# Kernel tuning notes

Hardware: AMD Instinct MI355X
Metric: run time of the kernel (lower is better)

Reference implementation:

```python
import jax, jax.numpy as jnp
import numpy as np

N_NODES = 40000
N_EDGES = 640000
D_IN = 128
D_OUT = 128
LN_EPS = 1e-5


def setup_inputs() -> dict:
    key = jax.random.key(0)
    ks = jax.random.split(key, 8)
    x = jax.random.normal(ks[0], (N_NODES, D_IN), dtype=jnp.float32)
    edge_index = jax.random.randint(ks[1], (2, N_EDGES), 0, N_NODES, dtype=jnp.int64)
    edge_weight_mean = jax.random.normal(ks[2], (N_EDGES,), dtype=jnp.float32)
    edge_weight_var = jax.random.uniform(ks[3], (N_EDGES,), dtype=jnp.float32)
    s = 1.0 / np.sqrt(D_IN)
    W_mean = jax.random.normal(ks[4], (D_IN, D_OUT), dtype=jnp.float32) * s
    b_mean = jax.random.normal(ks[5], (D_OUT,), dtype=jnp.float32) * 0.01
    W_logvar = jax.random.normal(ks[6], (D_IN, D_OUT), dtype=jnp.float32) * s
    b_logvar = jax.random.normal(ks[7], (D_OUT,), dtype=jnp.float32) * 0.01
    gamma = jnp.ones((D_OUT,), dtype=jnp.float32)
    beta = jnp.zeros((D_OUT,), dtype=jnp.float32)
    return {"x": x, "edge_index": edge_index, "edge_weight_mean": edge_weight_mean,
            "edge_weight_var": edge_weight_var, "W_mean": W_mean, "b_mean": b_mean,
            "W_logvar": W_logvar, "b_logvar": b_logvar, "gamma": gamma, "beta": beta}


def reference(x, edge_index, edge_weight_mean, edge_weight_var,
              W_mean, b_mean, W_logvar, b_logvar, gamma, beta):
    num_nodes = x.shape[0]
    h_mean = x @ W_mean + b_mean                      # [N, C]
    h_var = jnp.exp(x @ W_logvar + b_logvar)          # [N, C]
    row, col = edge_index[0], edge_index[1]
    ewm = edge_weight_mean[:, None]                   # [E, 1]
    ewv = edge_weight_var[:, None]                    # [E, 1]
    hm_c = h_mean[col]                                # gather [E, C]
    hv_c = h_var[col]
    msg_mean = hm_c * ewm
    msg_var = ewm ** 2 * hv_c + hm_c ** 2 * ewv
    out_mean = jax.ops.segment_sum(msg_mean, row, num_segments=num_nodes)
    out_var = jax.ops.segment_sum(msg_var, row, num_segments=num_nodes)
    degree = jax.ops.segment_sum(jnp.ones_like(edge_weight_mean), row, num_segments=num_nodes)
    degree = jnp.clip(degree, 1.0)[:, None]
    out_mean = out_mean / degree
    out_var = out_var / degree ** 2
    # LayerNorm over last dim (dropout is identity in eval mode)
    mu = jnp.mean(out_mean, axis=-1, keepdims=True)
    var = jnp.mean((out_mean - mu) ** 2, axis=-1, keepdims=True)
    out_mean = (out_mean - mu) * jax.lax.rsqrt(var + LN_EPS) * gamma + beta
    return (out_mean, out_var)
```

## Files before the change

kernel.cpp:

```cpp
#include <hip/hip_runtime.h>
#include <hip/hip_bf16.h>
#include <math.h>

#define N_NODES 40000
#define N_EDGES 640000
#define D 128
#define LN_EPS 1e-5f
#define STRIDE 48

typedef __attribute__((ext_vector_type(8))) short bf16x8;
typedef __attribute__((ext_vector_type(4))) float f32x4;

__device__ __forceinline__ unsigned bf2pack(float a, float b) {
    unsigned ua = __float_as_uint(a);
    ua = (ua + 0x7fffu + ((ua >> 16) & 1u)) >> 16;
    unsigned ub = __float_as_uint(b);
    ub = (ub + 0x7fffu + ((ub >> 16) & 1u)) >> 16;
    return ua | (ub << 16);
}
__device__ __forceinline__ unsigned short bfr(float a) {
    unsigned ua = __float_as_uint(a);
    return (unsigned short)((ua + 0x7fffu + ((ua >> 16) & 1u)) >> 16);
}
__device__ __forceinline__ float bflo(unsigned u) { return __uint_as_float(u << 16); }
__device__ __forceinline__ float bfhi(unsigned u) { return __uint_as_float(u & 0xffff0000u); }

__global__ __launch_bounds__(256) void packw_kernel(
    const float* __restrict__ Wm, const float* __restrict__ Wv,
    const float* __restrict__ bm, const float* __restrict__ bv,
    unsigned short* __restrict__ Wpk, float* __restrict__ bcat,
    int* __restrict__ counts)
{
    int idx = blockIdx.x * 256 + threadIdx.x;
    if (idx < N_NODES) counts[idx] = 0;
    if (idx < 256) bcat[idx] = (idx < 128) ? bm[idx] : bv[idx - 128];
    if (idx >= 32768) return;
    int j  = idx & 7;
    int l  = (idx >> 3) & 63;
    int nt = (idx >> 9) & 15;
    int kt = idx >> 13;
    int k = kt * 32 + (l >> 4) * 8 + j;
    int c = nt * 16 + (l & 15);
    float w = (c < 128) ? Wm[k * 128 + c] : Wv[k * 128 + (c - 128)];
    Wpk[idx] = bfr(w);
}

__global__ __launch_bounds__(256) void gemm_kernel(
    const float* __restrict__ x, const unsigned short* __restrict__ Wpk,
    const float* __restrict__ bcat, unsigned* __restrict__ hb,
    const int* __restrict__ row, int* __restrict__ counts,
    int* __restrict__ rank)
{
    const int gid = blockIdx.x * 256 + threadIdx.x;
    int4 r = ((const int4*)row)[gid];
    int k0 = atomicAdd(&counts[r.x], 1);
    int k1 = atomicAdd(&counts[r.y], 1);
    int k2 = atomicAdd(&counts[r.z], 1);
    int k3 = atomicAdd(&counts[r.w], 1);

    {
        const int w = threadIdx.x >> 6;
        const int l = threadIdx.x & 63;
        const int rbase = blockIdx.x * 64 + w * 16;
        const int arow = rbase + (l & 15);
        const int kqo = (l >> 4) * 8;

        bf16x8 a[4];
        #pragma unroll
        for (int kt = 0; kt < 4; ++kt) {
            const float* ap = &x[(size_t)arow * 128 + kt * 32 + kqo];
            float4 lo = *(const float4*)ap;
            float4 hi = *(const float4*)(ap + 4);
            uint4 au;
            au.x = bf2pack(lo.x, lo.y); au.y = bf2pack(lo.z, lo.w);
            au.z = bf2pack(hi.x, hi.y); au.w = bf2pack(hi.z, hi.w);
            a[kt] = *(bf16x8*)&au;
        }

        f32x4 acc[16];
        #pragma unroll
        for (int nt = 0; nt < 16; ++nt) acc[nt] = (f32x4){0.f, 0.f, 0.f, 0.f};

        const bf16x8* wp = (const bf16x8*)Wpk;
        #pragma unroll
        for (int kt = 0; kt < 4; ++kt) {
            #pragma unroll
            for (int nt = 0; nt < 16; ++nt) {
                bf16x8 b = wp[(kt * 16 + nt) * 64 + l];
                acc[nt] = __builtin_amdgcn_mfma_f32_16x16x32_bf16(a[kt], b, acc[nt], 0, 0, 0);
            }
        }

        const int c0 = l & 15;
        const int rq = rbase + (l >> 4) * 4;
        #pragma unroll
        for (int nt = 0; nt < 8; ++nt) {
            float bmv = bcat[nt * 16 + c0];
            float bvv = bcat[128 + nt * 16 + c0];
            #pragma unroll
            for (int q = 0; q < 4; ++q) {
                float m = acc[nt][q] + bmv;
                float v = expf(acc[nt + 8][q] + bvv);
                hb[(size_t)(rq + q) * 128 + nt * 16 + c0] = bf2pack(m, v);
            }
        }
    }

    ((int4*)rank)[gid] = make_int4(k0, k1, k2, k3);
}

__global__ __launch_bounds__(256) void scatter_kernel(
    const int* __restrict__ row, const int* __restrict__ col,
    const float* __restrict__ ewm, const float* __restrict__ ewv,
    const int* __restrict__ rank, uint2* __restrict__ ep8)
{
    int gid = blockIdx.x * 256 + threadIdx.x;
    int4   r  = ((const int4*)row)[gid];
    int4   c  = ((const int4*)col)[gid];
    int4   k  = ((const int4*)rank)[gid];
    float4 wm = ((const float4*)ewm)[gid];
    float4 wv = ((const float4*)ewv)[gid];

    if (k.x < STRIDE) ep8[(size_t)r.x * STRIDE + k.x] =
        make_uint2((unsigned)c.x, bf2pack(wm.x, wv.x));
    if (k.y < STRIDE) ep8[(size_t)r.y * STRIDE + k.y] =
        make_uint2((unsigned)c.y, bf2pack(wm.y, wv.y));
    if (k.z < STRIDE) ep8[(size_t)r.z * STRIDE + k.z] =
        make_uint2((unsigned)c.z, bf2pack(wm.z, wv.z));
    if (k.w < STRIDE) ep8[(size_t)r.w * STRIDE + k.w] =
        make_uint2((unsigned)c.w, bf2pack(wm.w, wv.w));
}

__device__ __forceinline__ void accum_edge(
    const uint4& h, float wm, float wv, float (&am)[4], float (&av)[4])
{
    float wm2 = wm * wm;
    float mf, vf;
    mf = bflo(h.x); vf = bfhi(h.x);
    am[0] = fmaf(mf, wm, am[0]);
    av[0] = fmaf(wm2, vf, fmaf(mf * mf, wv, av[0]));
    mf = bflo(h.y); vf = bfhi(h.y);
    am[1] = fmaf(mf, wm, am[1]);
    av[1] = fmaf(wm2, vf, fmaf(mf * mf, wv, av[1]));
    mf = bflo(h.z); vf = bfhi(h.z);
    am[2] = fmaf(mf, wm, am[2]);
    av[2] = fmaf(wm2, vf, fmaf(mf * mf, wv, av[2]));
    mf = bflo(h.w); vf = bfhi(h.w);
    am[3] = fmaf(mf, wm, am[3]);
    av[3] = fmaf(wm2, vf, fmaf(mf * mf, wv, av[3]));
}

__global__ __launch_bounds__(256) void agg_kernel(
    const uint4* __restrict__ hb, const int* __restrict__ counts,
    const uint2* __restrict__ ep8,
    const float* __restrict__ gamma, const float* __restrict__ beta,
    float* __restrict__ out)
{
    const int wid  = threadIdx.x >> 6;
    const int lane = threadIdx.x & 63;
    const int half = lane >> 5;
    const int sub  = lane & 31;
    const int n = blockIdx.x * 4 + wid;

    const int start = n * STRIDE;
    int cnt = counts[n];
    const int end = start + (cnt < STRIDE ? cnt : STRIDE);

    float am[4] = {}, av[4] = {};

    int e = start;
    for (; e + 8 <= end; e += 8) {
        uint2 m[4]; uint4 h[4];
        #pragma unroll
        for (int i = 0; i < 4; ++i) m[i] = ep8[e + 2 * i + half];
        #pragma unroll
        for (int i = 0; i < 4; ++i)
            h[i] = hb[(size_t)m[i].x * 32 + sub];
        #pragma unroll
        for (int i = 0; i < 4; ++i)
            accum_edge(h[i], bflo(m[i].y), bfhi(m[i].y), am, av);
    }
    for (; e + 2 <= end; e += 2) {
        uint2 m = ep8[e + half];
        uint4 h = hb[(size_t)m.x * 32 + sub];
        accum_edge(h, bflo(m.y), bfhi(m.y), am, av);
    }
    if (e < end && half == 0) {
        uint2 m = ep8[e];
        uint4 h = hb[(size_t)m.x * 32 + sub];
        accum_edge(h, bflo(m.y), bfhi(m.y), am, av);
    }

    #pragma unroll
    for (int j = 0; j < 4; ++j) {
        am[j] += __shfl_xor(am[j], 32);
        av[j] += __shfl_xor(av[j], 32);
    }

    float degi = 1.0f / fmaxf((float)(end - start), 1.0f);
    float dg2 = degi * degi;
    #pragma unroll
    for (int j = 0; j < 4; ++j) { am[j] *= degi; av[j] *= dg2; }

    float s = am[0] + am[1] + am[2] + am[3];
    #pragma unroll
    for (int off = 16; off >= 1; off >>= 1) s += __shfl_xor(s, off);
    float mu = s * (1.0f / 128.0f);
    float d0 = am[0] - mu, d1 = am[1] - mu, d2 = am[2] - mu, d3 = am[3] - mu;
    float q = d0 * d0 + d1 * d1 + d2 * d2 + d3 * d3;
    #pragma unroll
    for (int off = 16; off >= 1; off >>= 1) q += __shfl_xor(q, off);
    float var = q * (1.0f / 128.0f);
    float rs = rsqrtf(var + LN_EPS);

    if (half == 0) {
        float4 g = *(const float4*)&gamma[sub * 4];
        float4 b = *(const float4*)&beta[sub * 4];
        float4 om = make_float4(fmaf(d0 * rs, g.x, b.x), fmaf(d1 * rs, g.y, b.y),
                                fmaf(d2 * rs, g.z, b.z), fmaf(d3 * rs, g.w, b.w));
        *(float4*)&out[(size_t)n * D + sub * 4] = om;
        *(float4*)&out[(size_t)N_NODES * D + (size_t)n * D + sub * 4] =
            make_float4(av[0], av[1], av[2], av[3]);
    }
}

extern "C" void kernel_launch(void* const* d_in, const int* in_sizes, int n_in,
                              void* d_out, int out_size, void* d_ws, size_t ws_size,
                              hipStream_t stream)
{
    const float* x     = (const float*)d_in[0];
    const int*   eidx  = (const int*)d_in[1];
    const float* ewm   = (const float*)d_in[2];
    const float* ewv   = (const float*)d_in[3];
    const float* Wm    = (const float*)d_in[4];
    const float* bm    = (const float*)d_in[5];
    const float* Wv    = (const float*)d_in[6];
    const float* bv    = (const float*)d_in[7];
    const float* gamma = (const float*)d_in[8];
    const float* beta  = (const float*)d_in[9];
    const int* row = eidx;
    const int* col = eidx + N_EDGES;

    char* ws = (char*)d_ws;
    size_t off = 0;
    auto alloc = [&](size_t bytes) {
        void* p = ws + off;
        off += (bytes + 255) & ~(size_t)255;
        return p;
    };
    unsigned* hb        = (unsigned*)alloc((size_t)N_NODES * 512);
    unsigned short* Wpk = (unsigned short*)alloc(32768 * 2);
    float* bcat    = (float*)alloc(256 * 4);
    int*   counts  = (int*)alloc((size_t)N_NODES * 4);
    int*   rank    = (int*)alloc((size_t)N_EDGES * 4);
    uint2* ep8     = (uint2*)alloc((size_t)N_NODES * STRIDE * 8);

    packw_kernel<<<160, 256, 0, stream>>>(Wm, Wv, bm, bv, Wpk, bcat, counts);
    gemm_kernel<<<N_NODES / 64, 256, 0, stream>>>(x, Wpk, bcat, hb, row, counts, rank);
    scatter_kernel<<<N_EDGES / 4 / 256, 256, 0, stream>>>(
        row, col, ewm, ewv, rank, ep8);
    agg_kernel<<<N_NODES / 4, 256, 0, stream>>>(
        (const uint4*)hb, counts, ep8, gamma, beta, (float*)d_out);
}
```

Baseline: 105.7 us.

## Slice feature table by 16-column blocks and split aggregation from LayerNorm

The packed h table is stored transposed into 8 feature slices, each holding 16 columns for every node. Aggregation now runs one grid block per (node group, slice), so each slice's gather working set (about 2.5 MB) can stay in cache. LayerNorm moves to a separate kernel that rereads the mean output. The cost is 8x more edge-list reads, 4-byte instead of 16-byte gathers, and an extra launch plus an extra round trip of the mean output through memory.

```diff
diff --git a/kernel.cpp b/kernel.cpp
--- a/kernel.cpp
+++ b/kernel.cpp
@@ -47,7 +47,7 @@
 
 __global__ __launch_bounds__(256) void gemm_kernel(
     const float* __restrict__ x, const unsigned short* __restrict__ Wpk,
-    const float* __restrict__ bcat, unsigned* __restrict__ hb,
+    const float* __restrict__ bcat, unsigned* __restrict__ hbT,
     const int* __restrict__ row, int* __restrict__ counts,
     int* __restrict__ rank)
 {
@@ -101,7 +101,8 @@
             for (int q = 0; q < 4; ++q) {
                 float m = acc[nt][q] + bmv;
                 float v = expf(acc[nt + 8][q] + bvv);
-                hb[(size_t)(rq + q) * 128 + nt * 16 + c0] = bf2pack(m, v);
+                hbT[(size_t)nt * (N_NODES * 16) + (size_t)(rq + q) * 16 + c0] =
+                    bf2pack(m, v);
             }
         }
     }
@@ -131,97 +132,71 @@
         make_uint2((unsigned)c.w, bf2pack(wm.w, wv.w));
 }
 
-__device__ __forceinline__ void accum_edge(
-    const uint4& h, float wm, float wv, float (&am)[4], float (&av)[4])
-{
-    float wm2 = wm * wm;
-    float mf, vf;
-    mf = bflo(h.x); vf = bfhi(h.x);
-    am[0] = fmaf(mf, wm, am[0]);
-    av[0] = fmaf(wm2, vf, fmaf(mf * mf, wv, av[0]));
-    mf = bflo(h.y); vf = bfhi(h.y);
-    am[1] = fmaf(mf, wm, am[1]);
-    av[1] = fmaf(wm2, vf, fmaf(mf * mf, wv, av[1]));
-    mf = bflo(h.z); vf = bfhi(h.z);
-    am[2] = fmaf(mf, wm, am[2]);
-    av[2] = fmaf(wm2, vf, fmaf(mf * mf, wv, av[2]));
-    mf = bflo(h.w); vf = bfhi(h.w);
-    am[3] = fmaf(mf, wm, am[3]);
-    av[3] = fmaf(wm2, vf, fmaf(mf * mf, wv, av[3]));
-}
-
-__global__ __launch_bounds__(256) void agg_kernel(
-    const uint4* __restrict__ hb, const int* __restrict__ counts,
-    const uint2* __restrict__ ep8,
+__global__ __launch_bounds__(256) void aggA_kernel(
+    const unsigned* __restrict__ hbT, const int* __restrict__ counts,
+    const uint2* __restrict__ ep8, float* __restrict__ out)
+{
+    const int wv   = threadIdx.x >> 6;
+    const int lane = threadIdx.x & 63;
+    const int fl   = lane & 15;
+    const int eg   = lane >> 4;
+    const int slice = blockIdx.x & 7;
+    const int n = (blockIdx.x >> 3) * 4 + wv;
+
+    const int start = n * STRIDE;
+    int cnt = counts[n];
+    cnt = cnt < STRIDE ? cnt : STRIDE;
+    const int end = start + cnt;
+
+    const unsigned* hs = hbT + (size_t)slice * (N_NODES * 16);
+
+    float am = 0.f, av = 0.f;
+    for (int e = start + eg; e < end; e += 4) {
+        uint2 m = ep8[e];
+        unsigned h = hs[(size_t)m.x * 16 + fl];
+        float hm = bflo(h), hv = bfhi(h);
+        float wm = bflo(m.y), wvv = bfhi(m.y);
+        am = fmaf(hm, wm, am);
+        av = fmaf(wm * wm, hv, fmaf(hm * hm, wvv, av));
+    }
+    am += __shfl_xor(am, 16); am += __shfl_xor(am, 32);
+    av += __shfl_xor(av, 16); av += __shfl_xor(av, 32);
+
+    float degi = 1.0f / fmaxf((float)cnt, 1.0f);
+    am *= degi;
+    av *= degi * degi;
+
+    if (eg == 0) {
+        int feat = slice * 16 + fl;
+        out[(size_t)n * D + feat] = am;
+        out[(size_t)N_NODES * D + (size_t)n * D + feat] = av;
+    }
+}
+
+__global__ __launch_bounds__(256) void aggB_kernel(
     const float* __restrict__ gamma, const float* __restrict__ beta,
     float* __restrict__ out)
 {
-    const int wid  = threadIdx.x >> 6;
+    const int wv = threadIdx.x >> 6;
     const int lane = threadIdx.x & 63;
-    const int half = lane >> 5;
-    const int sub  = lane & 31;
-    const int n = blockIdx.x * 4 + wid;
-
-    const int start = n * STRIDE;
-    int cnt = counts[n];
-    const int end = start + (cnt < STRIDE ? cnt : STRIDE);
-
-    float am[4] = {}, av[4] = {};
-
-    int e = start;
-    for (; e + 8 <= end; e += 8) {
-        uint2 m[4]; uint4 h[4];
-        #pragma unroll
-        for (int i = 0; i < 4; ++i) m[i] = ep8[e + 2 * i + half];
-        #pragma unroll
-        for (int i = 0; i < 4; ++i)
-            h[i] = hb[(size_t)m[i].x * 32 + sub];
-        #pragma unroll
-        for (int i = 0; i < 4; ++i)
-            accum_edge(h[i], bflo(m[i].y), bfhi(m[i].y), am, av);
-    }
-    for (; e + 2 <= end; e += 2) {
-        uint2 m = ep8[e + half];
-        uint4 h = hb[(size_t)m.x * 32 + sub];
-        accum_edge(h, bflo(m.y), bfhi(m.y), am, av);
-    }
-    if (e < end && half == 0) {
-        uint2 m = ep8[e];
-        uint4 h = hb[(size_t)m.x * 32 + sub];
-        accum_edge(h, bflo(m.y), bfhi(m.y), am, av);
-    }
-
+    const int n = blockIdx.x * 4 + wv;
+
+    float2 a = *(const float2*)&out[(size_t)n * D + lane * 2];
+    float s = a.x + a.y;
     #pragma unroll
-    for (int j = 0; j < 4; ++j) {
-        am[j] += __shfl_xor(am[j], 32);
-        av[j] += __shfl_xor(av[j], 32);
-    }
-
-    float degi = 1.0f / fmaxf((float)(end - start), 1.0f);
-    float dg2 = degi * degi;
+    for (int off = 32; off >= 1; off >>= 1) s += __shfl_xor(s, off);
+    float mu = s * (1.0f / 128.0f);
+    float d0 = a.x - mu, d1 = a.y - mu;
+    float q = d0 * d0 + d1 * d1;
     #pragma unroll
-    for (int j = 0; j < 4; ++j) { am[j] *= degi; av[j] *= dg2; }
-
-    float s = am[0] + am[1] + am[2] + am[3];
-    #pragma unroll
-    for (int off = 16; off >= 1; off >>= 1) s += __shfl_xor(s, off);
-    float mu = s * (1.0f / 128.0f);
-    float d0 = am[0] - mu, d1 = am[1] - mu, d2 = am[2] - mu, d3 = am[3] - mu;
-    float q = d0 * d0 + d1 * d1 + d2 * d2 + d3 * d3;
-    #pragma unroll
-    for (int off = 16; off >= 1; off >>= 1) q += __shfl_xor(q, off);
+    for (int off = 32; off >= 1; off >>= 1) q += __shfl_xor(q, off);
     float var = q * (1.0f / 128.0f);
     float rs = rsqrtf(var + LN_EPS);
 
-    if (half == 0) {
-        float4 g = *(const float4*)&gamma[sub * 4];
-        float4 b = *(const float4*)&beta[sub * 4];
-        float4 om = make_float4(fmaf(d0 * rs, g.x, b.x), fmaf(d1 * rs, g.y, b.y),
-                                fmaf(d2 * rs, g.z, b.z), fmaf(d3 * rs, g.w, b.w));
-        *(float4*)&out[(size_t)n * D + sub * 4] = om;
-        *(float4*)&out[(size_t)N_NODES * D + (size_t)n * D + sub * 4] =
-            make_float4(av[0], av[1], av[2], av[3]);
-    }
+    float2 g = *(const float2*)&gamma[lane * 2];
+    float2 b = *(const float2*)&beta[lane * 2];
+    *(float2*)&out[(size_t)n * D + lane * 2] =
+        make_float2(fmaf(d0 * rs, g.x, b.x), fmaf(d1 * rs, g.y, b.y));
 }
 
 extern "C" void kernel_launch(void* const* d_in, const int* in_sizes, int n_in,
@@ -248,7 +223,7 @@
         off += (bytes + 255) & ~(size_t)255;
         return p;
     };
-    unsigned* hb        = (unsigned*)alloc((size_t)N_NODES * 512);
+    unsigned* hbT       = (unsigned*)alloc((size_t)N_NODES * 512);
     unsigned short* Wpk = (unsigned short*)alloc(32768 * 2);
     float* bcat    = (float*)alloc(256 * 4);
     int*   counts  = (int*)alloc((size_t)N_NODES * 4);
@@ -256,9 +231,10 @@
     uint2* ep8     = (uint2*)alloc((size_t)N_NODES * STRIDE * 8);
 
     packw_kernel<<<160, 256, 0, stream>>>(Wm, Wv, bm, bv, Wpk, bcat, counts);
-    gemm_kernel<<<N_NODES / 64, 256, 0, stream>>>(x, Wpk, bcat, hb, row, counts, rank);
+    gemm_kernel<<<N_NODES / 64, 256, 0, stream>>>(x, Wpk, bcat, hbT, row, counts, rank);
     scatter_kernel<<<N_EDGES / 4 / 256, 256, 0, stream>>>(
         row, col, ewm, ewv, rank, ep8);
-    agg_kernel<<<N_NODES / 4, 256, 0, stream>>>(
-        (const uint4*)hb, counts, ep8, gamma, beta, (float*)d_out);
-}
+    aggA_kernel<<<(N_NODES / 4) * 8, 256, 0, stream>>>(
+        hbT, counts, ep8, (float*)d_out);
+    aggB_kernel<<<N_NODES / 4, 256, 0, stream>>>(gamma, beta, (float*)d_out);
+}
```

New measurement: 204.7 us. +93.6%, slower.

## Fuse edge scatter into GEMM kernel and store fp32 edge weights in float4 packs

Applied to the files above, without the earlier changes.

The separate scatter kernel is folded into the GEMM kernel: each thread now handles two edges, takes their slot ranks via atomics and immediately writes the CSR-like edge record, so the rank buffer round trip and one launch disappear. The GEMM grid is doubled to 1250 blocks of 32 rows, with each wave computing half of the output columns for both mean and logvar. Edge records grow from 8-byte packed bf16 to 16-byte float4 with full-precision weights, which doubles the edge traffic in the aggregation kernel but removes the bf16 rounding of the weights.

```diff
diff --git a/kernel.cpp b/kernel.cpp
--- a/kernel.cpp
+++ b/kernel.cpp
@@ -48,20 +48,20 @@
 __global__ __launch_bounds__(256) void gemm_kernel(
     const float* __restrict__ x, const unsigned short* __restrict__ Wpk,
     const float* __restrict__ bcat, unsigned* __restrict__ hb,
-    const int* __restrict__ row, int* __restrict__ counts,
-    int* __restrict__ rank)
+    const int* __restrict__ row, const int* __restrict__ col,
+    const float* __restrict__ ewm, const float* __restrict__ ewv,
+    int* __restrict__ counts, float4* __restrict__ epack)
 {
     const int gid = blockIdx.x * 256 + threadIdx.x;
-    int4 r = ((const int4*)row)[gid];
+    int2 r = ((const int2*)row)[gid];
     int k0 = atomicAdd(&counts[r.x], 1);
     int k1 = atomicAdd(&counts[r.y], 1);
-    int k2 = atomicAdd(&counts[r.z], 1);
-    int k3 = atomicAdd(&counts[r.w], 1);
 
     {
         const int w = threadIdx.x >> 6;
         const int l = threadIdx.x & 63;
-        const int rbase = blockIdx.x * 64 + w * 16;
+        const int rbase = blockIdx.x * 32 + (w & 1) * 16;
+        const int colh = w >> 1;
         const int arow = rbase + (l & 15);
         const int kqo = (l >> 4) * 8;
 
@@ -77,58 +77,52 @@
             a[kt] = *(bf16x8*)&au;
         }
 
-        f32x4 acc[16];
-        #pragma unroll
-        for (int nt = 0; nt < 16; ++nt) acc[nt] = (f32x4){0.f, 0.f, 0.f, 0.f};
+        f32x4 accm[4], accv[4];
+        #pragma unroll
+        for (int i = 0; i < 4; ++i) {
+            accm[i] = (f32x4){0.f, 0.f, 0.f, 0.f};
+            accv[i] = (f32x4){0.f, 0.f, 0.f, 0.f};
+        }
 
         const bf16x8* wp = (const bf16x8*)Wpk;
         #pragma unroll
         for (int kt = 0; kt < 4; ++kt) {
             #pragma unroll
-            for (int nt = 0; nt < 16; ++nt) {
-                bf16x8 b = wp[(kt * 16 + nt) * 64 + l];
-                acc[nt] = __builtin_amdgcn_mfma_f32_16x16x32_bf16(a[kt], b, acc[nt], 0, 0, 0);
+            for (int i = 0; i < 4; ++i) {
+                int ntm = colh * 4 + i;
+                int ntv = 8 + colh * 4 + i;
+                bf16x8 bmf = wp[(kt * 16 + ntm) * 64 + l];
+                bf16x8 bvf = wp[(kt * 16 + ntv) * 64 + l];
+                accm[i] = __builtin_amdgcn_mfma_f32_16x16x32_bf16(a[kt], bmf, accm[i], 0, 0, 0);
+                accv[i] = __builtin_amdgcn_mfma_f32_16x16x32_bf16(a[kt], bvf, accv[i], 0, 0, 0);
             }
         }
 
         const int c0 = l & 15;
         const int rq = rbase + (l >> 4) * 4;
         #pragma unroll
-        for (int nt = 0; nt < 8; ++nt) {
-            float bmv = bcat[nt * 16 + c0];
-            float bvv = bcat[128 + nt * 16 + c0];
+        for (int i = 0; i < 4; ++i) {
+            int feat = colh * 64 + i * 16 + c0;
+            float bmv = bcat[feat];
+            float bvv = bcat[128 + feat];
             #pragma unroll
             for (int q = 0; q < 4; ++q) {
-                float m = acc[nt][q] + bmv;
-                float v = expf(acc[nt + 8][q] + bvv);
-                hb[(size_t)(rq + q) * 128 + nt * 16 + c0] = bf2pack(m, v);
+                float m = accm[i][q] + bmv;
+                float v = expf(accv[i][q] + bvv);
+                hb[(size_t)(rq + q) * 128 + feat] = bf2pack(m, v);
             }
         }
     }
 
-    ((int4*)rank)[gid] = make_int4(k0, k1, k2, k3);
-}
-
-__global__ __launch_bounds__(256) void scatter_kernel(
-    const int* __restrict__ row, const int* __restrict__ col,
-    const float* __restrict__ ewm, const float* __restrict__ ewv,
-    const int* __restrict__ rank, uint2* __restrict__ ep8)
-{
-    int gid = blockIdx.x * 256 + threadIdx.x;
-    int4   r  = ((const int4*)row)[gid];
-    int4   c  = ((const int4*)col)[gid];
-    int4   k  = ((const int4*)rank)[gid];
-    float4 wm = ((const float4*)ewm)[gid];
-    float4 wv = ((const float4*)ewv)[gid];
-
-    if (k.x < STRIDE) ep8[(size_t)r.x * STRIDE + k.x] =
-        make_uint2((unsigned)c.x, bf2pack(wm.x, wv.x));
-    if (k.y < STRIDE) ep8[(size_t)r.y * STRIDE + k.y] =
-        make_uint2((unsigned)c.y, bf2pack(wm.y, wv.y));
-    if (k.z < STRIDE) ep8[(size_t)r.z * STRIDE + k.z] =
-        make_uint2((unsigned)c.z, bf2pack(wm.z, wv.z));
-    if (k.w < STRIDE) ep8[(size_t)r.w * STRIDE + k.w] =
-        make_uint2((unsigned)c.w, bf2pack(wm.w, wv.w));
+    {
+        int2   c2 = ((const int2*)col)[gid];
+        float2 wm = ((const float2*)ewm)[gid];
+        float2 wv = ((const float2*)ewv)[gid];
+        if (k0 < STRIDE) epack[(size_t)r.x * STRIDE + k0] =
+            make_float4(__int_as_float(c2.x), wm.x, wv.x, 0.0f);
+        if (k1 < STRIDE) epack[(size_t)r.y * STRIDE + k1] =
+            make_float4(__int_as_float(c2.y), wm.y, wv.y, 0.0f);
+    }
 }
 
 __device__ __forceinline__ void accum_edge(
@@ -152,7 +146,7 @@
 
 __global__ __launch_bounds__(256) void agg_kernel(
     const uint4* __restrict__ hb, const int* __restrict__ counts,
-    const uint2* __restrict__ ep8,
+    const float4* __restrict__ epack,
     const float* __restrict__ gamma, const float* __restrict__ beta,
     float* __restrict__ out)
 {
@@ -164,31 +158,35 @@
 
     const int start = n * STRIDE;
     int cnt = counts[n];
-    const int end = start + (cnt < STRIDE ? cnt : STRIDE);
+    cnt = cnt < STRIDE ? cnt : STRIDE;
+    const int end = start + cnt;
 
     float am[4] = {}, av[4] = {};
 
     int e = start;
     for (; e + 8 <= end; e += 8) {
-        uint2 m[4]; uint4 h[4];
-        #pragma unroll
-        for (int i = 0; i < 4; ++i) m[i] = ep8[e + 2 * i + half];
-        #pragma unroll
-        for (int i = 0; i < 4; ++i)
-            h[i] = hb[(size_t)m[i].x * 32 + sub];
-        #pragma unroll
-        for (int i = 0; i < 4; ++i)
-            accum_edge(h[i], bflo(m[i].y), bfhi(m[i].y), am, av);
+        float4 m[4]; uint4 h[4];
+        #pragma unroll
+        for (int i = 0; i < 4; ++i) m[i] = epack[e + 2 * i + half];
+        #pragma unroll
+        for (int i = 0; i < 4; ++i) {
+            int c = __float_as_int(m[i].x);
+            h[i] = hb[(size_t)c * 32 + sub];
+        }
+        #pragma unroll
+        for (int i = 0; i < 4; ++i) accum_edge(h[i], m[i].y, m[i].z, am, av);
     }
     for (; e + 2 <= end; e += 2) {
-        uint2 m = ep8[e + half];
-        uint4 h = hb[(size_t)m.x * 32 + sub];
-        accum_edge(h, bflo(m.y), bfhi(m.y), am, av);
+        float4 m = epack[e + half];
+        int c = __float_as_int(m.x);
+        uint4 h = hb[(size_t)c * 32 + sub];
+        accum_edge(h, m.y, m.z, am, av);
     }
     if (e < end && half == 0) {
-        uint2 m = ep8[e];
-        uint4 h = hb[(size_t)m.x * 32 + sub];
-        accum_edge(h, bflo(m.y), bfhi(m.y), am, av);
+        float4 m = epack[e];
+        int c = __float_as_int(m.x);
+        uint4 h = hb[(size_t)c * 32 + sub];
+        accum_edge(h, m.y, m.z, am, av);
     }
 
     #pragma unroll
@@ -197,7 +195,7 @@
         av[j] += __shfl_xor(av[j], 32);
     }
 
-    float degi = 1.0f / fmaxf((float)(end - start), 1.0f);
+    float degi = 1.0f / fmaxf((float)cnt, 1.0f);
     float dg2 = degi * degi;
     #pragma unroll
     for (int j = 0; j < 4; ++j) { am[j] *= degi; av[j] *= dg2; }
@@ -252,13 +250,11 @@
     unsigned short* Wpk = (unsigned short*)alloc(32768 * 2);
     float* bcat    = (float*)alloc(256 * 4);
     int*   counts  = (int*)alloc((size_t)N_NODES * 4);
-    int*   rank    = (int*)alloc((size_t)N_EDGES * 4);
-    uint2* ep8     = (uint2*)alloc((size_t)N_NODES * STRIDE * 8);
+    float4* epack  = (float4*)alloc((size_t)N_NODES * STRIDE * 16);
 
     packw_kernel<<<160, 256, 0, stream>>>(Wm, Wv, bm, bv, Wpk, bcat, counts);
-    gemm_kernel<<<N_NODES / 64, 256, 0, stream>>>(x, Wpk, bcat, hb, row, counts, rank);
-    scatter_kernel<<<N_EDGES / 4 / 256, 256, 0, stream>>>(
-        row, col, ewm, ewv, rank, ep8);
+    gemm_kernel<<<1250, 256, 0, stream>>>(
+        x, Wpk, bcat, hb, row, col, ewm, ewv, counts, epack);
     agg_kernel<<<N_NODES / 4, 256, 0, stream>>>(
-        (const uint4*)hb, counts, ep8, gamma, beta, (float*)d_out);
-}
+        (const uint4*)hb, counts, epack, gamma, beta, (float*)d_out);
+}
```

Result: faster. 93.22 us (-11.8%).
